# Optimization experiments

Measured on AMD Instinct MI355X. Metric: run time of the kernel, lower is better.

## Reference

```python
import jax, jax.numpy as jnp
import numpy as np

BETA = 0.25

def setup_inputs() -> dict:
    key = jax.random.key(0)
    k1, k2 = jax.random.split(key)
    N, K, D = 262144, 256, 256
    z_e = jax.random.normal(k1, (N, D), dtype=jnp.float32)
    # nn.Embedding init: uniform(-1/K, 1/K)
    emb_weight = jax.random.uniform(k2, (K, D), dtype=jnp.float32, minval=-1.0 / K, maxval=1.0 / K)
    return {"z_e": z_e, "emb_weight": emb_weight}

def reference(z_e, emb_weight):
    # squared L2 distances: ||z||^2 + ||e||^2 - 2 z e^T  -> [N, K]
    dist = (jnp.sum(z_e ** 2, axis=1, keepdims=True)
            + jnp.sum(emb_weight ** 2, axis=1)
            - 2.0 * jnp.matmul(z_e, emb_weight.T))
    encoding_inds = jnp.argmin(dist, axis=1)  # [N]
    z_q = emb_weight[encoding_inds]           # [N, D]

    sg = jax.lax.stop_gradient
    commitment_loss = jnp.mean((sg(z_e) - z_q) ** 2)
    codebook_loss = jnp.mean((z_e - sg(z_q)) ** 2)
    loss = codebook_loss + BETA * commitment_loss

    # straight-through estimator
    z_q_st = z_e + sg(z_q - z_e)
    return z_q_st, encoding_inds, loss
```

## Files before the change

### kernel.cpp

```cpp
#include <hip/hip_runtime.h>

typedef __attribute__((ext_vector_type(8))) short bf16x8;
typedef __attribute__((ext_vector_type(4))) float f32x4;
typedef __attribute__((ext_vector_type(4))) unsigned short us4;
typedef __attribute__((ext_vector_type(8))) unsigned short us8;

#define NROWS 262144
#define KC 256
#define DD 256
#define BM 128
#define DK 32
#define TAU 1.5e-3f
#define FCAP 65536

__device__ __forceinline__ float np_pw128_sq(const float* a) {
    float r[8];
#pragma unroll
    for (int j = 0; j < 8; ++j) r[j] = __fmul_rn(a[j], a[j]);
    for (int i = 8; i < 128; i += 8) {
#pragma unroll
        for (int j = 0; j < 8; ++j)
            r[j] = __fadd_rn(r[j], __fmul_rn(a[i + j], a[i + j]));
    }
    float t01 = __fadd_rn(r[0], r[1]), t23 = __fadd_rn(r[2], r[3]);
    float t45 = __fadd_rn(r[4], r[5]), t67 = __fadd_rn(r[6], r[7]);
    return __fadd_rn(__fadd_rn(t01, t23), __fadd_rn(t45, t67));
}
__device__ __forceinline__ float np_sum256_sq(const float* a) {
    return __fadd_rn(np_pw128_sq(a), np_pw128_sq(a + 128));
}

__device__ __forceinline__ unsigned short bf16_rne(float x) {
    unsigned b = __float_as_uint(x);
    b += 0x7FFFu + ((b >> 16) & 1u);
    return (unsigned short)(b >> 16);
}

__global__ void vq_prep(const float* __restrict__ emb, float* __restrict__ se,
                        double* __restrict__ accum, int* __restrict__ gcnt) {
    int k = threadIdx.x;
    if (k == 0) { *accum = 0.0; *gcnt = 0; }
    se[k] = np_sum256_sq(emb + (size_t)k * DD);
}

__global__ void vq_split(const float* __restrict__ emb, unsigned short* __restrict__ ph) {
    int f = (blockIdx.x * 256 + threadIdx.x) * 4;
    float4 v = *reinterpret_cast<const float4*>(emb + f);
    int k = f >> 8, d = f & 255;
    int off = (d >> 5) * (KC * DK) + k * DK + (d & 31);
    us4 h;
    h[0] = bf16_rne(v.x); h[1] = bf16_rne(v.y);
    h[2] = bf16_rne(v.z); h[3] = bf16_rne(v.w);
    *reinterpret_cast<us4*>(ph + off) = h;
}

__global__ __launch_bounds__(256, 2)
void vq_main(const float* __restrict__ ze, const unsigned short* __restrict__ ph,
             const float* __restrict__ se_g, float* __restrict__ out_inds,
             double* __restrict__ accum, int* __restrict__ glist, int* __restrict__ gcnt)
{
    __shared__ float se_s[KC];
    __shared__ float wv1[4 * 16], wv2[4 * 16];
    __shared__ int   wk1[4 * 16];
    __shared__ float red[256];

    const int t = threadIdx.x;
    const int w = t >> 6;
    const int q = (t >> 4) & 3;
    const int c = t & 15;
    const size_t m0 = (size_t)blockIdx.x * BM;

    se_s[t] = se_g[t];

    bf16x8 bfr[4][8];
#pragma unroll
    for (int nf = 0; nf < 4; ++nf)
#pragma unroll
        for (int dci = 0; dci < 8; ++dci)
            bfr[nf][dci] = *reinterpret_cast<const bf16x8*>(
                ph + dci * (KC * DK) + (w * 64 + nf * 16 + c) * DK + q * 8);

    __syncthreads();

    float sz_run = 0.f, loss_run = 0.f;

    float4 z0[8], z1[8];
    {
        const float* zb = ze + (m0 + c) * DD + q * 8;
#pragma unroll
        for (int dci = 0; dci < 8; ++dci) {
            z0[dci] = *reinterpret_cast<const float4*>(zb + dci * 32);
            z1[dci] = *reinterpret_cast<const float4*>(zb + dci * 32 + 4);
        }
    }

    for (int step = 0; step < BM / 16; ++step) {
        f32x4 acc[4];
#pragma unroll
        for (int nf = 0; nf < 4; ++nf) acc[nf] = (f32x4){0.f, 0.f, 0.f, 0.f};
#pragma unroll
        for (int dci = 0; dci < 8; ++dci) {
            float4 a = z0[dci], b = z1[dci];
            if (w == 0) {
                sz_run = fmaf(a.x, a.x, sz_run); sz_run = fmaf(a.y, a.y, sz_run);
                sz_run = fmaf(a.z, a.z, sz_run); sz_run = fmaf(a.w, a.w, sz_run);
                sz_run = fmaf(b.x, b.x, sz_run); sz_run = fmaf(b.y, b.y, sz_run);
                sz_run = fmaf(b.z, b.z, sz_run); sz_run = fmaf(b.w, b.w, sz_run);
            }
            us8 h;
            h[0] = bf16_rne(a.x); h[1] = bf16_rne(a.y); h[2] = bf16_rne(a.z); h[3] = bf16_rne(a.w);
            h[4] = bf16_rne(b.x); h[5] = bf16_rne(b.y); h[6] = bf16_rne(b.z); h[7] = bf16_rne(b.w);
            bf16x8 af = __builtin_bit_cast(bf16x8, h);
#pragma unroll
            for (int nf = 0; nf < 4; ++nf)
                acc[nf] = __builtin_amdgcn_mfma_f32_16x16x32_bf16(af, bfr[nf][dci], acc[nf], 0, 0, 0);
        }
        if (step < BM / 16 - 1) {
            const float* zb = ze + (m0 + (step + 1) * 16 + c) * DD + q * 8;
#pragma unroll
            for (int dci = 0; dci < 8; ++dci) {
                z0[dci] = *reinterpret_cast<const float4*>(zb + dci * 32);
                z1[dci] = *reinterpret_cast<const float4*>(zb + dci * 32 + 4);
            }
        }

#pragma unroll
        for (int j = 0; j < 4; ++j) {
            float v1 = 3.4e38f, v2 = 3.4e38f; int k1 = 0x7fffffff;
#pragma unroll
            for (int nf = 0; nf < 4; ++nf) {
                int k = 64 * w + 16 * nf + c;
                float dv = fmaf(-2.f, acc[nf][j], se_s[k]);
                if (dv < v1) { v2 = v1; v1 = dv; k1 = k; }
                else if (dv < v2) { v2 = dv; }
            }
#pragma unroll
            for (int off = 1; off < 16; off <<= 1) {
                float ov1 = __shfl_xor(v1, off, 64);
                float ov2 = __shfl_xor(v2, off, 64);
                int   ok1 = __shfl_xor(k1, off, 64);
                bool other = (ov1 < v1) || (ov1 == v1 && ok1 < k1);
                float nv2 = other ? fminf(v1, ov2) : fminf(v2, ov1);
                if (other) { v1 = ov1; k1 = ok1; }
                v2 = nv2;
            }
            if (c == 0) {
                wv1[w * 16 + 4 * q + j] = v1;
                wv2[w * 16 + 4 * q + j] = v2;
                wk1[w * 16 + 4 * q + j] = k1;
            }
        }
        __syncthreads();

        if (t < 16) {
            float v1 = wv1[t], v2 = wv2[t]; int k1 = wk1[t];
#pragma unroll
            for (int ww = 1; ww < 4; ++ww) {
                float ov1 = wv1[ww * 16 + t], ov2 = wv2[ww * 16 + t];
                int ok1 = wk1[ww * 16 + t];
                bool other = (ov1 < v1) || (ov1 == v1 && ok1 < k1);
                float nv2 = other ? fminf(v1, ov2) : fminf(v2, ov1);
                if (other) { v1 = ov1; k1 = ok1; }
                v2 = nv2;
            }
            out_inds[m0 + step * 16 + t] = (float)k1;
            loss_run += v1;
            if (v2 - v1 < TAU) {
                int s_ = atomicAdd(gcnt, 1);
                if (s_ < FCAP) glist[s_] = (int)(m0 + step * 16 + t);
            }
        }
        __syncthreads();
    }

    red[t] = (w == 0 ? sz_run : 0.f) + (t < 16 ? loss_run : 0.f);
    __syncthreads();
    for (int s = 128; s > 0; s >>= 1) {
        if (t < s) red[t] += red[t + s];
        __syncthreads();
    }
    if (t == 0) atomicAdd(accum, (double)red[0]);
}

__global__ __launch_bounds__(256)
void vq_fix(const float* __restrict__ ze, const float* __restrict__ emb,
            const float* __restrict__ se_g, const int* __restrict__ glist,
            const int* __restrict__ gcnt, float* __restrict__ out_inds)
{
    __shared__ float dq[16][256];
    __shared__ float srow_s[16];
    __shared__ int   rowid_s[16];

    const int t = threadIdx.x;
    int F = *gcnt; if (F > FCAP) F = FCAP;
    const float se_k = se_g[t];
    const float4* e4p = reinterpret_cast<const float4*>(emb + (size_t)t * DD);

    for (int g = blockIdx.x * 16; g < F; g += gridDim.x * 16) {
        __syncthreads();
        if (t < 16) {
            int idx = g + t; if (idx > F - 1) idx = F - 1;
            int row = glist[idx];
            rowid_s[t] = row;
            srow_s[t] = np_sum256_sq(ze + (size_t)row * DD);
        }
        __syncthreads();

        const float* zp[16];
#pragma unroll
        for (int r = 0; r < 16; ++r)
            zp[r] = ze + (size_t)__builtin_amdgcn_readfirstlane(rowid_s[r]) * DD;

        float m32[16];
#pragma unroll
        for (int r = 0; r < 16; ++r) m32[r] = 0.f;
        for (int d4 = 0; d4 < 64; ++d4) {
            float4 e4 = e4p[d4];
            const int d = d4 * 4;
#pragma unroll
            for (int r = 0; r < 16; ++r) {
                m32[r] = __fmaf_rn(zp[r][d + 0], e4.x, m32[r]);
                m32[r] = __fmaf_rn(zp[r][d + 1], e4.y, m32[r]);
                m32[r] = __fmaf_rn(zp[r][d + 2], e4.z, m32[r]);
                m32[r] = __fmaf_rn(zp[r][d + 3], e4.w, m32[r]);
            }
        }
#pragma unroll
        for (int r = 0; r < 16; ++r) {
            float A = __fadd_rn(srow_s[r], se_k);
            dq[r][t] = __fsub_rn(A, __fmul_rn(2.0f, m32[r]));
        }
        __syncthreads();

        {
            const int r = t >> 4, p = t & 15;
            float bv = 3.4e38f; int bk = 0x7fffffff;
#pragma unroll
            for (int i = 0; i < 16; ++i) {
                int k = p * 16 + i;
                float v = dq[r][k];
                if (v < bv) { bv = v; bk = k; }
            }
#pragma unroll
            for (int off = 1; off < 16; off <<= 1) {
                float ov = __shfl_xor(bv, off, 64);
                int   ok = __shfl_xor(bk, off, 64);
                if (ov < bv || (ov == bv && ok < bk)) { bv = ov; bk = ok; }
            }
            if (p == 0 && g + r < F) out_inds[rowid_s[r]] = (float)bk;
        }
        __syncthreads();
    }
}

__global__ __launch_bounds__(256)
void vq_gather(const float* __restrict__ emb, const float* __restrict__ out_inds,
               float* __restrict__ out_zq)
{
    const int t = threadIdx.x;
    const int w = t >> 6, l = t & 63;
    const size_t m0 = (size_t)blockIdx.x * 128 + (size_t)w * 32;
#pragma unroll 8
    for (int r = 0; r < 32; ++r) {
        int k = (int)out_inds[m0 + r];
        float4 v = *reinterpret_cast<const float4*>(emb + (size_t)k * DD + l * 4);
        *reinterpret_cast<float4*>(out_zq + (m0 + r) * DD + l * 4) = v;
    }
}

__global__ void vq_fin(const double* __restrict__ accum, float* __restrict__ out_loss) {
    *out_loss = (float)(1.25 * (*accum) / ((double)NROWS * (double)DD));
}

extern "C" void kernel_launch(void* const* d_in, const int* in_sizes, int n_in,
                              void* d_out, int out_size, void* d_ws, size_t ws_size,
                              hipStream_t stream) {
    const float* ze  = (const float*)d_in[0];
    const float* emb = (const float*)d_in[1];
    float* out      = (float*)d_out;
    float* out_zq   = out;
    float* out_inds = out + (size_t)NROWS * DD;
    float* out_loss = out + (size_t)NROWS * DD + NROWS;

    double* accum = (double*)d_ws;
    int*    gcnt  = (int*)((char*)d_ws + 8);
    float*  se    = (float*)((char*)d_ws + 256);
    int*    glist = (int*)((char*)d_ws + 4096);
    unsigned short* ph = (unsigned short*)((char*)d_ws + 4096 + 262144);

    vq_prep<<<1, 256, 0, stream>>>(emb, se, accum, gcnt);
    vq_split<<<KC * DD / (256 * 4), 256, 0, stream>>>(emb, ph);
    vq_main<<<NROWS / BM, 256, 0, stream>>>(ze, ph, se, out_inds, accum, glist, gcnt);
    vq_fix<<<1024, 256, 0, stream>>>(ze, emb, se, glist, gcnt, out_inds);
    vq_gather<<<NROWS / 128, 256, 0, stream>>>(emb, out_inds, out_zq);
    vq_fin<<<1, 1, 0, stream>>>(accum, out_loss);
}
```

Baseline: 347.6 us.

## Defer cross-wave argmin merge to end of block, removing per-step barriers

Per-wave top-2 results for all 128 rows go into larger shared arrays, and one final cross-wave merge by 128 threads replaces the per-16-row merge, which needed two __syncthreads per step. The bf16 conversion of z is split from the MFMA chain, so the next rows' loads are issued before the matrix multiplies. Codebook norms are cached in registers instead of being reread from LDS. This costs extra shared memory and registers (afrag), which may affect occupancy at 2 blocks per CU.

```diff
diff --git a/kernel.cpp b/kernel.cpp
--- a/kernel.cpp
+++ b/kernel.cpp
@@ -60,8 +60,8 @@
              double* __restrict__ accum, int* __restrict__ glist, int* __restrict__ gcnt)
 {
     __shared__ float se_s[KC];
-    __shared__ float wv1[4 * 16], wv2[4 * 16];
-    __shared__ int   wk1[4 * 16];
+    __shared__ float wv1[4 * BM], wv2[4 * BM];
+    __shared__ int   wk1[4 * BM];
     __shared__ float red[256];
 
     const int t = threadIdx.x;
@@ -82,7 +82,11 @@
 
     __syncthreads();
 
-    float sz_run = 0.f, loss_run = 0.f;
+    float se_v[4];
+#pragma unroll
+    for (int nf = 0; nf < 4; ++nf) se_v[nf] = se_s[64 * w + 16 * nf + c];
+
+    float sz_run = 0.f;
 
     float4 z0[8], z1[8];
     {
@@ -95,9 +99,7 @@
     }
 
     for (int step = 0; step < BM / 16; ++step) {
-        f32x4 acc[4];
-#pragma unroll
-        for (int nf = 0; nf < 4; ++nf) acc[nf] = (f32x4){0.f, 0.f, 0.f, 0.f};
+        bf16x8 afrag[8];
 #pragma unroll
         for (int dci = 0; dci < 8; ++dci) {
             float4 a = z0[dci], b = z1[dci];
@@ -110,10 +112,7 @@
             us8 h;
             h[0] = bf16_rne(a.x); h[1] = bf16_rne(a.y); h[2] = bf16_rne(a.z); h[3] = bf16_rne(a.w);
             h[4] = bf16_rne(b.x); h[5] = bf16_rne(b.y); h[6] = bf16_rne(b.z); h[7] = bf16_rne(b.w);
-            bf16x8 af = __builtin_bit_cast(bf16x8, h);
-#pragma unroll
-            for (int nf = 0; nf < 4; ++nf)
-                acc[nf] = __builtin_amdgcn_mfma_f32_16x16x32_bf16(af, bfr[nf][dci], acc[nf], 0, 0, 0);
+            afrag[dci] = __builtin_bit_cast(bf16x8, h);
         }
         if (step < BM / 16 - 1) {
             const float* zb = ze + (m0 + (step + 1) * 16 + c) * DD + q * 8;
@@ -123,6 +122,14 @@
                 z1[dci] = *reinterpret_cast<const float4*>(zb + dci * 32 + 4);
             }
         }
+        f32x4 acc[4];
+#pragma unroll
+        for (int nf = 0; nf < 4; ++nf) acc[nf] = (f32x4){0.f, 0.f, 0.f, 0.f};
+#pragma unroll
+        for (int dci = 0; dci < 8; ++dci)
+#pragma unroll
+            for (int nf = 0; nf < 4; ++nf)
+                acc[nf] = __builtin_amdgcn_mfma_f32_16x16x32_bf16(afrag[dci], bfr[nf][dci], acc[nf], 0, 0, 0);
 
 #pragma unroll
         for (int j = 0; j < 4; ++j) {
@@ -130,7 +137,7 @@
 #pragma unroll
             for (int nf = 0; nf < 4; ++nf) {
                 int k = 64 * w + 16 * nf + c;
-                float dv = fmaf(-2.f, acc[nf][j], se_s[k]);
+                float dv = fmaf(-2.f, acc[nf][j], se_v[nf]);
                 if (dv < v1) { v2 = v1; v1 = dv; k1 = k; }
                 else if (dv < v2) { v2 = dv; }
             }
@@ -145,35 +152,37 @@
                 v2 = nv2;
             }
             if (c == 0) {
-                wv1[w * 16 + 4 * q + j] = v1;
-                wv2[w * 16 + 4 * q + j] = v2;
-                wk1[w * 16 + 4 * q + j] = k1;
-            }
-        }
-        __syncthreads();
-
-        if (t < 16) {
-            float v1 = wv1[t], v2 = wv2[t]; int k1 = wk1[t];
-#pragma unroll
-            for (int ww = 1; ww < 4; ++ww) {
-                float ov1 = wv1[ww * 16 + t], ov2 = wv2[ww * 16 + t];
-                int ok1 = wk1[ww * 16 + t];
-                bool other = (ov1 < v1) || (ov1 == v1 && ok1 < k1);
-                float nv2 = other ? fminf(v1, ov2) : fminf(v2, ov1);
-                if (other) { v1 = ov1; k1 = ok1; }
-                v2 = nv2;
-            }
-            out_inds[m0 + step * 16 + t] = (float)k1;
-            loss_run += v1;
-            if (v2 - v1 < TAU) {
-                int s_ = atomicAdd(gcnt, 1);
-                if (s_ < FCAP) glist[s_] = (int)(m0 + step * 16 + t);
-            }
-        }
-        __syncthreads();
-    }
-
-    red[t] = (w == 0 ? sz_run : 0.f) + (t < 16 ? loss_run : 0.f);
+                int row = step * 16 + 4 * q + j;
+                wv1[w * BM + row] = v1;
+                wv2[w * BM + row] = v2;
+                wk1[w * BM + row] = k1;
+            }
+        }
+    }
+    __syncthreads();
+
+    float lossv = 0.f;
+    if (t < BM) {
+        float v1 = wv1[t], v2 = wv2[t]; int k1 = wk1[t];
+#pragma unroll
+        for (int ww = 1; ww < 4; ++ww) {
+            float ov1 = wv1[ww * BM + t], ov2 = wv2[ww * BM + t];
+            int ok1 = wk1[ww * BM + t];
+            bool other = (ov1 < v1) || (ov1 == v1 && ok1 < k1);
+            float nv2 = other ? fminf(v1, ov2) : fminf(v2, ov1);
+            if (other) { v1 = ov1; k1 = ok1; }
+            v2 = nv2;
+        }
+        out_inds[m0 + t] = (float)k1;
+        lossv = v1;
+        if (v2 - v1 < TAU) {
+            int s_ = atomicAdd(gcnt, 1);
+            if (s_ < FCAP) glist[s_] = (int)(m0 + t);
+        }
+    }
+    __syncthreads();
+
+    red[t] = (w == 0 ? sz_run : 0.f) + (t < BM ? lossv : 0.f);
     __syncthreads();
     for (int s = 128; s > 0; s >>= 1) {
         if (t < s) red[t] += red[t + s];
```

New measurement: 383.2 us. 1.1x slower.
